# Kernel optimization log

Hardware: AMD Instinct MI355X
Metric: run time of the kernel (lower is better)

The kernel has to match this reference:

```python
import jax, jax.numpy as jnp
import numpy as np

HEADS = 4  # from init_kwargs

def _branch_index(seq_len: int) -> jnp.ndarray:
    # position 0 -> layer_s(0), 1 -> layer_r(1), 2 -> layer_o(2),
    # then alternating layer_a(3)/layer_v(4) starting at position 3.
    tail = jnp.where((jnp.arange(seq_len - 3) % 2) == 0, 3, 4)
    return jnp.concatenate([jnp.array([0, 1, 2], dtype=tail.dtype), tail])


def setup_inputs() -> dict:
    key = jax.random.key(0)
    k1, k2, k3 = jax.random.split(key, 3)
    B, S, H = 128, 513, 256
    x = jax.random.normal(k1, (B, S, H), dtype=jnp.float32)
    # 5 Linear layers, nn.Linear convention: y = x @ W.T + b, W: [out,in]
    W = jax.random.normal(k2, (5, H, H), dtype=jnp.float32) * (1.0 / np.sqrt(H))
    b = jax.random.normal(k3, (5, H), dtype=jnp.float32) * 0.02
    return {"x": x, "W": W, "b": b}


def reference(x, W, b):
    # Original applies each Linear to a position-masked copy of x and sums.
    # Since the 5 masks are disjoint one-hots over positions, the weight term
    # at position t is x[t] @ W[m(t)].T; the bias term is sum of ALL 5 biases
    # (Linear(0) = bias), applied at every position.
    B, S, H = x.shape
    idx = _branch_index(S)            # [S] in {0..4}
    Wsel = W[idx]
    out = jnp.einsum('bsh,sdh->bsd', x, Wsel) + b.sum(axis=0)
    return out.reshape(B, S, HEADS, H // HEADS)
```

## Files before the change

kernel.cpp:

```cpp
#include <hip/hip_runtime.h>
#include <hip/hip_bf16.h>

#define B_ 128
#define S_ 513
#define H_ 256
#define SH_ (S_ * H_)

typedef __attribute__((ext_vector_type(8))) short short8;
typedef __attribute__((ext_vector_type(4))) float f32x4;

static __device__ inline short8 pack8(float4 a, float4 b) {
    union { short8 s; __hip_bfloat162 h[4]; } u;
    u.h[0] = __float22bfloat162_rn(make_float2(a.x, a.y));
    u.h[1] = __float22bfloat162_rn(make_float2(a.z, a.w));
    u.h[2] = __float22bfloat162_rn(make_float2(b.x, b.y));
    u.h[3] = __float22bfloat162_rn(make_float2(b.z, b.w));
    return u.s;
}

__global__ void prep_kernel(const float* __restrict__ W,
                            const float* __restrict__ bias,
                            unsigned short* __restrict__ Wbf,
                            float* __restrict__ bsum) {
    int t = blockIdx.x * 256 + threadIdx.x;
    if (t < 5 * 32 * 256) {
        int m  = t >> 13;
        int r  = t & 8191;
        int d  = r >> 5;
        int kc = r & 31;
        const float* src = W + (((size_t)m * 256 + d) * 256 + kc * 8);
        float4 v0 = *(const float4*)src;
        float4 v1 = *(const float4*)(src + 4);
        *(short8*)(Wbf + ((size_t)(m * 32 + kc) * 256 + d) * 8) = pack8(v0, v1);
    }
    if (t < H_) {
        float s = 0.f;
#pragma unroll
        for (int i = 0; i < 5; ++i) s += bias[i * H_ + t];
        bsum[t] = s;
    }
}

template <int MODE>
__global__ __launch_bounds__(256, 6)
void sel_gemm_kernel(const float* __restrict__ x,
                     const void* __restrict__ Wp,
                     const void* __restrict__ bp,
                     float* __restrict__ out) {
    const int s     = blockIdx.x >> 2;
    const int qtr   = blockIdx.x & 3;
    const int m_idx = (s < 3) ? s : ((s & 1) ? 3 : 4);

    __shared__ unsigned short As[32 * 256];

    const int t    = threadIdx.x;
    const int lane = t & 63;
    const int w    = t >> 6;
    const int lrow = lane & 15;
    const int quad = lane >> 4;

    const float* xs = x + (size_t)s * H_ + (size_t)qtr * 32 * SH_;
#pragma unroll
    for (int i = 0; i < 4; ++i) {
        int flat = i * 256 + t;
        int r = flat >> 5;
        int c = flat & 31;
        const float* src = xs + (size_t)r * SH_ + c * 8;
        float4 v0 = *(const float4*)src;
        float4 v1 = *(const float4*)(src + 4);
        *(short8*)&As[r * 256 + ((c ^ (r & 7)) * 8)] = pack8(v0, v1);
    }

    f32x4 acc[2][4];
#pragma unroll
    for (int i = 0; i < 2; ++i)
#pragma unroll
        for (int j = 0; j < 4; ++j) {
            f32x4 z = {0.f, 0.f, 0.f, 0.f};
            acc[i][j] = z;
        }

    __syncthreads();

#pragma unroll
    for (int kk = 0; kk < 8; ++kk) {
        short8 xfr[2];
        const int cc = kk * 4 + quad;
#pragma unroll
        for (int i = 0; i < 2; ++i) {
            const int r = i * 16 + lrow;
            xfr[i] = *(const short8*)&As[r * 256 + ((cc ^ (r & 7)) * 8)];
        }

#pragma unroll
        for (int j = 0; j < 4; ++j) {
            short8 wfr;
            if (MODE == 0) {
                const unsigned short* Wk =
                    (const unsigned short*)Wp +
                    ((size_t)(m_idx * 32 + kk * 4 + quad) * 256) * 8;
                wfr = *(const short8*)(Wk + (size_t)(w * 64 + j * 16 + lrow) * 8);
            } else {
                const float* Wb = (const float*)Wp + (size_t)m_idx * H_ * H_;
                const float* wrow = Wb + (size_t)(w * 64 + j * 16 + lrow) * H_
                                    + kk * 32 + quad * 8;
                float4 v0 = *(const float4*)wrow;
                float4 v1 = *(const float4*)(wrow + 4);
                wfr = pack8(v0, v1);
            }
#pragma unroll
            for (int i = 0; i < 2; ++i)
                acc[i][j] = __builtin_amdgcn_mfma_f32_16x16x32_bf16(
                    wfr, xfr[i], acc[i][j], 0, 0, 0);
        }
    }

#pragma unroll
    for (int j = 0; j < 4; ++j) {
        const int d0 = w * 64 + j * 16 + quad * 4;
        f32x4 bj;
        if (MODE == 0) {
            bj = *(const f32x4*)((const float*)bp + d0);
        } else {
            const float* bias = (const float*)bp;
#pragma unroll
            for (int r = 0; r < 4; ++r) {
                float sum = 0.f;
#pragma unroll
                for (int i = 0; i < 5; ++i) sum += bias[i * H_ + d0 + r];
                bj[r] = sum;
            }
        }
#pragma unroll
        for (int i = 0; i < 2; ++i) {
            const int b = qtr * 32 + i * 16 + lrow;
            f32x4 v = acc[i][j] + bj;
            *(f32x4*)(out + ((size_t)b * S_ + s) * H_ + d0) = v;
        }
    }
}

extern "C" void kernel_launch(void* const* d_in, const int* in_sizes, int n_in,
                              void* d_out, int out_size, void* d_ws, size_t ws_size,
                              hipStream_t stream) {
    const float* x    = (const float*)d_in[0];
    const float* W    = (const float*)d_in[1];
    const float* bias = (const float*)d_in[2];
    float* out = (float*)d_out;

    const size_t w_elems  = (size_t)5 * H_ * H_;
    const size_t ws_need  = w_elems * sizeof(unsigned short) + H_ * sizeof(float);

    if (ws_size >= ws_need) {
        unsigned short* Wbf = (unsigned short*)d_ws;
        float* bsum = (float*)((char*)d_ws + w_elems * sizeof(unsigned short));
        prep_kernel<<<dim3(160), dim3(256), 0, stream>>>(W, bias, Wbf, bsum);
        sel_gemm_kernel<0><<<dim3(4 * S_), dim3(256), 0, stream>>>(
            x, (const void*)Wbf, (const void*)bsum, out);
    } else {
        sel_gemm_kernel<1><<<dim3(4 * S_), dim3(256), 0, stream>>>(
            x, (const void*)W, (const void*)bias, out);
    }
}
```

Measured before the change: 134.7 us.

## Use single-wave blocks loading x directly to registers, drop LDS staging

Each block becomes a single 64-thread wavefront covering 32 batch rows by 128 output columns, so the grid doubles in size. x fragments are loaded straight from global memory into registers and converted to bf16, which removes the shared-memory staging and the barrier. Output stores become nontemporal. In exchange, each x row is now read by two blocks instead of one, and each wave holds twice as many accumulators.

```diff
diff --git a/kernel.cpp b/kernel.cpp
--- a/kernel.cpp
+++ b/kernel.cpp
@@ -42,68 +42,58 @@
 }
 
 template <int MODE>
-__global__ __launch_bounds__(256, 6)
+__global__ __launch_bounds__(64, 4)
 void sel_gemm_kernel(const float* __restrict__ x,
                      const void* __restrict__ Wp,
                      const void* __restrict__ bp,
                      float* __restrict__ out) {
-    const int s     = blockIdx.x >> 2;
-    const int qtr   = blockIdx.x & 3;
+    const int bid = blockIdx.x;
+    const int s   = bid >> 3;
+    const int r3  = bid & 7;
+    const int bg  = (r3 & 3) * 32;
+    const int dh  = (r3 >> 2) * 128;
     const int m_idx = (s < 3) ? s : ((s & 1) ? 3 : 4);
 
-    __shared__ unsigned short As[32 * 256];
-
-    const int t    = threadIdx.x;
-    const int lane = t & 63;
-    const int w    = t >> 6;
+    const int lane = threadIdx.x & 63;
     const int lrow = lane & 15;
     const int quad = lane >> 4;
 
-    const float* xs = x + (size_t)s * H_ + (size_t)qtr * 32 * SH_;
-#pragma unroll
-    for (int i = 0; i < 4; ++i) {
-        int flat = i * 256 + t;
-        int r = flat >> 5;
-        int c = flat & 31;
-        const float* src = xs + (size_t)r * SH_ + c * 8;
-        float4 v0 = *(const float4*)src;
-        float4 v1 = *(const float4*)(src + 4);
-        *(short8*)&As[r * 256 + ((c ^ (r & 7)) * 8)] = pack8(v0, v1);
-    }
-
-    f32x4 acc[2][4];
+    f32x4 acc[2][8];
 #pragma unroll
     for (int i = 0; i < 2; ++i)
 #pragma unroll
-        for (int j = 0; j < 4; ++j) {
+        for (int j = 0; j < 8; ++j) {
             f32x4 z = {0.f, 0.f, 0.f, 0.f};
             acc[i][j] = z;
         }
 
-    __syncthreads();
+    const float* xb = x + (size_t)s * H_;
 
 #pragma unroll
     for (int kk = 0; kk < 8; ++kk) {
         short8 xfr[2];
-        const int cc = kk * 4 + quad;
 #pragma unroll
         for (int i = 0; i < 2; ++i) {
-            const int r = i * 16 + lrow;
-            xfr[i] = *(const short8*)&As[r * 256 + ((cc ^ (r & 7)) * 8)];
+            const float* src =
+                xb + (size_t)(bg + i * 16 + lrow) * SH_ + kk * 32 + quad * 8;
+            float4 v0 = *(const float4*)src;
+            float4 v1 = *(const float4*)(src + 4);
+            xfr[i] = pack8(v0, v1);
         }
 
 #pragma unroll
-        for (int j = 0; j < 4; ++j) {
+        for (int j = 0; j < 8; ++j) {
             short8 wfr;
             if (MODE == 0) {
                 const unsigned short* Wk =
                     (const unsigned short*)Wp +
-                    ((size_t)(m_idx * 32 + kk * 4 + quad) * 256) * 8;
-                wfr = *(const short8*)(Wk + (size_t)(w * 64 + j * 16 + lrow) * 8);
+                    ((size_t)(m_idx * 32 + kk * 4 + quad) * 256 +
+                     (dh + j * 16 + lrow)) * 8;
+                wfr = *(const short8*)Wk;
             } else {
-                const float* Wb = (const float*)Wp + (size_t)m_idx * H_ * H_;
-                const float* wrow = Wb + (size_t)(w * 64 + j * 16 + lrow) * H_
-                                    + kk * 32 + quad * 8;
+                const float* wrow = (const float*)Wp +
+                    (size_t)m_idx * H_ * H_ +
+                    (size_t)(dh + j * 16 + lrow) * H_ + kk * 32 + quad * 8;
                 float4 v0 = *(const float4*)wrow;
                 float4 v1 = *(const float4*)(wrow + 4);
                 wfr = pack8(v0, v1);
@@ -116,8 +106,8 @@
     }
 
 #pragma unroll
-    for (int j = 0; j < 4; ++j) {
-        const int d0 = w * 64 + j * 16 + quad * 4;
+    for (int j = 0; j < 8; ++j) {
+        const int d0 = dh + j * 16 + quad * 4;
         f32x4 bj;
         if (MODE == 0) {
             bj = *(const f32x4*)((const float*)bp + d0);
@@ -133,9 +123,10 @@
         }
 #pragma unroll
         for (int i = 0; i < 2; ++i) {
-            const int b = qtr * 32 + i * 16 + lrow;
+            const int b = bg + i * 16 + lrow;
             f32x4 v = acc[i][j] + bj;
-            *(f32x4*)(out + ((size_t)b * S_ + s) * H_ + d0) = v;
+            __builtin_nontemporal_store(
+                v, (f32x4*)(out + ((size_t)b * S_ + s) * H_ + d0));
         }
     }
 }
@@ -155,10 +146,10 @@
         unsigned short* Wbf = (unsigned short*)d_ws;
         float* bsum = (float*)((char*)d_ws + w_elems * sizeof(unsigned short));
         prep_kernel<<<dim3(160), dim3(256), 0, stream>>>(W, bias, Wbf, bsum);
-        sel_gemm_kernel<0><<<dim3(4 * S_), dim3(256), 0, stream>>>(
+        sel_gemm_kernel<0><<<dim3(8 * S_), dim3(64), 0, stream>>>(
             x, (const void*)Wbf, (const void*)bsum, out);
     } else {
-        sel_gemm_kernel<1><<<dim3(4 * S_), dim3(256), 0, stream>>>(
+        sel_gemm_kernel<1><<<dim3(8 * S_), dim3(64), 0, stream>>>(
             x, (const void*)W, (const void*)bias, out);
     }
 }
```

New measurement: 173.8 us. 1.29x slower.
